# Kernel optimization log

Hardware: AMD Instinct MI355X
Metric: run time of the kernel (lower is better)

The kernel has to match this reference:

```python
import jax, jax.numpy as jnp
import numpy as np

N, K, D = 65536, 1024, 512


def setup_inputs() -> dict:
    key = jax.random.key(0)
    k1, k2, k3 = jax.random.split(key, 3)
    x = jax.random.normal(k1, (N, D), dtype=jnp.float32)
    y = jax.random.randint(k2, (N,), 0, K)  # true/assigned cluster labels
    centers = jax.random.normal(k3, (K, D), dtype=jnp.float32)  # nn.Parameter
    return {"x": x, "y": y, "centers": centers}


def reference(x, y, centers):
    # caldis: squared euclidean distance from every point to every center.
    # original expand+sub+square+sum without materializing [N, K, D]).
    x2 = jnp.sum(x * x, axis=1, keepdims=True)          # [N, 1]
    c2 = jnp.sum(centers * centers, axis=1)              # [K]
    distance = x2 - 2.0 * (x @ centers.T) + c2           # [N, K]

    # predict: torch.sort(distance)[1][:, 0] == index of the smallest distance
    ynew = jnp.argmin(distance, axis=1)                  # [N]

    # calwei + calloss: one-hot(y) * distance summed == gather distance[i, y[i]]
    loss = jnp.sum(jnp.take_along_axis(distance, y[:, None], axis=1))

    return loss, ynew
```

## Files before the change

### kernel.cpp

```cpp
#include <hip/hip_runtime.h>

#define NPTS 65536
#define KC   1024
#define DD   512

using bf16x8 = __attribute__((ext_vector_type(8))) __bf16;
using f32x4  = __attribute__((ext_vector_type(4))) float;

__device__ __forceinline__ void gld_lds16(const void* g, void* lds_base) {
  __builtin_amdgcn_global_load_lds(
      (const __attribute__((address_space(1))) unsigned int*)(uintptr_t)g,
      (__attribute__((address_space(3))) unsigned int*)(unsigned int)(uintptr_t)lds_base,
      16, 0, 0);
}

__device__ __forceinline__ uint2 pack4(const float4& v) {
  uint2 r;
  r.x = (__float_as_uint(v.x) >> 16) | (__float_as_uint(v.y) & 0xffff0000u);
  r.y = (__float_as_uint(v.z) >> 16) | (__float_as_uint(v.w) & 0xffff0000u);
  return r;
}


__global__ __launch_bounds__(256) void prep_kernel(
    const float* __restrict__ x, const int* __restrict__ y,
    const float* __restrict__ centers, uint4* __restrict__ xb,
    uint4* __restrict__ cbT, float* __restrict__ c2,
    float* __restrict__ partial) {
  const int w = threadIdx.x >> 6, l = threadIdx.x & 63;
  if (blockIdx.x >= 4096) {
    const int row = (blockIdx.x - 4096) * 4 + w;
    const float4* cf4 = (const float4*)centers;
    float4 a = cf4[row * 128 + 2 * l];
    float4 b = cf4[row * 128 + 2 * l + 1];
    uint2 pa = pack4(a), pb = pack4(b);
    cbT[(l >> 2) * 4096 + row * 4 + (l & 3)] = make_uint4(pa.x, pa.y, pb.x, pb.y);
    float s = a.x * a.x + a.y * a.y + a.z * a.z + a.w * a.w +
              b.x * b.x + b.y * b.y + b.z * b.z + b.w * b.w;
#pragma unroll
    for (int off = 32; off; off >>= 1) s += __shfl_down(s, off, 64);
    if (l == 0) c2[row] = s;
    return;
  }
  const int rbase = blockIdx.x * 16 + w * 4;
  const float4* xr = (const float4*)(x + (size_t)rbase * DD);
  float4 a[4], b[4];
#pragma unroll
  for (int r = 0; r < 4; r++) {
    a[r] = xr[r * 128 + 2 * l];
    b[r] = xr[r * 128 + 2 * l + 1];
  }
  int yr[4];
#pragma unroll
  for (int r = 0; r < 4; r++) yr[r] = y[rbase + r];
  float4 ca[4], cb4[4];
#pragma unroll
  for (int r = 0; r < 4; r++) {
    const float4* cr = (const float4*)(centers + (size_t)yr[r] * DD);
    ca[r]  = cr[2 * l];
    cb4[r] = cr[2 * l + 1];
  }
#pragma unroll
  for (int r = 0; r < 4; r++) {
    uint2 pa = pack4(a[r]), pb = pack4(b[r]);
    xb[(size_t)(rbase + r) * 64 + l] = make_uint4(pa.x, pa.y, pb.x, pb.y);
  }
  float s = 0.f;
#pragma unroll
  for (int r = 0; r < 4; r++) {
    float d0 = a[r].x - ca[r].x, d1 = a[r].y - ca[r].y;
    float d2 = a[r].z - ca[r].z, d3 = a[r].w - ca[r].w;
    float d4 = b[r].x - cb4[r].x, d5 = b[r].y - cb4[r].y;
    float d6 = b[r].z - cb4[r].z, d7 = b[r].w - cb4[r].w;
    s += d0 * d0 + d1 * d1 + d2 * d2 + d3 * d3 +
         d4 * d4 + d5 * d5 + d6 * d6 + d7 * d7;
  }
#pragma unroll
  for (int off = 32; off; off >>= 1) s += __shfl_down(s, off, 64);
  __shared__ float ps[4];
  if (l == 0) ps[w] = s;
  __syncthreads();
  if (threadIdx.x == 0) partial[blockIdx.x] = ps[0] + ps[1] + ps[2] + ps[3];
}

__global__ __launch_bounds__(512, 2) void gemm_argmin(
    const uint4* __restrict__ xb, const uint4* __restrict__ cbT,
    const float* __restrict__ c2, const float* __restrict__ partial,
    float* __restrict__ loss_out, float* __restrict__ ynew_out) {
  __shared__ uint4 As[8192];
  __shared__ float c2s[KC];
  __shared__ float ls[8];

  const int t = threadIdx.x;
  const int w = t >> 6, l = t & 63;
  const int wm = w >> 2, wn = w & 3;
  const int q4 = l >> 4, m16 = l & 15;
  const int row0 = blockIdx.x * 128;

  c2s[t] = c2[t];
  c2s[t + 512] = c2[t + 512];

  const int srow = l >> 2;
  const int schk = (l & 3) ^ ((l >> 3) & 3);
  const uint4* aB = xb + ((size_t)(row0 + w * 16 + srow) * 64 + schk);
  const int xs = q4 ^ ((m16 >> 1) & 3);
  const int al0 = (wm * 64 + m16) * 4 + xs;
  const int bl0 = (wn * 64 + m16) * 4 + q4;

#pragma unroll
  for (int p = 0; p < 4; p++)
    gld_lds16(aB + p * 4, &As[p * 512 + w * 64]);

  bf16x8 bA[4], bB[4];
#pragma unroll
  for (int j = 0; j < 4; j++)
    bA[j] = *(const bf16x8*)(cbT + bl0 + j * 64);

  f32x4 acc[4][4];
#pragma unroll
  for (int i = 0; i < 4; i++)
#pragma unroll
    for (int j = 0; j < 4; j++) acc[i][j] = (f32x4){0.f, 0.f, 0.f, 0.f};

  float best[16];
  int bi_[16];
#pragma unroll
  for (int i = 0; i < 16; i++) { best[i] = 3.4e38f; bi_[i] = 0; }

  asm volatile("s_waitcnt vmcnt(7)" ::: "memory");
  __builtin_amdgcn_s_barrier();

#define FOLD(P)                                                             \
  {                                                                         \
    const int n0f = (P) * 256;                                              \
    _Pragma("unroll")                                                       \
    for (int j = 0; j < 4; j++) {                                           \
      const int n = n0f + wn * 64 + j * 16 + m16;                           \
      const float cc = c2s[n];                                              \
      _Pragma("unroll")                                                     \
      for (int i = 0; i < 4; i++)                                           \
        _Pragma("unroll")                                                   \
        for (int r = 0; r < 4; r++) {                                       \
          float v = fmaf(-2.f, acc[i][j][r], cc);                           \
          const int bidx = i * 4 + r;                                       \
          if (v < best[bidx]) { best[bidx] = v; bi_[bidx] = n; }            \
          acc[i][j][r] = 0.f;                                               \
        }                                                                   \
    }                                                                       \
  }

#define TILE_P0(T, BC, BN)                                                  \
  {                                                                         \
    const int kt = (T) & 15;                                                \
    if ((T) < 15) {                                                         \
      const uint4* bp = cbT + ((T) + 1) * 4096;                             \
      _Pragma("unroll")                                                     \
      for (int j = 0; j < 4; j++)                                           \
        BN[j] = *(const bf16x8*)(bp + bl0 + j * 64);                        \
    }                                                                       \
    if ((T) < 12)                                                           \
      gld_lds16(aB + ((T) + 4) * 4, &As[((T) + 4) * 512 + w * 64]);         \
    bf16x8 af[4];                                                           \
    _Pragma("unroll")                                                       \
    for (int i = 0; i < 4; i++)                                             \
      af[i] = *(const bf16x8*)&As[kt * 512 + al0 + i * 64];                 \
    _Pragma("unroll")                                                       \
    for (int j = 0; j < 4; j++)                                             \
      _Pragma("unroll")                                                     \
      for (int i = 0; i < 4; i++)                                           \
        acc[i][j] = __builtin_amdgcn_mfma_f32_16x16x32_bf16(af[i], BC[j], acc[i][j], 0, 0, 0); \
    if ((T) == 15) FOLD(0);                                                 \
    if ((T) < 12) asm volatile("s_waitcnt vmcnt(1)" ::: "memory");          \
    else          asm volatile("s_waitcnt vmcnt(0)" ::: "memory");          \
    __builtin_amdgcn_s_barrier();                                           \
  }

#pragma unroll 1
  for (int s = 0; s < 8; ++s) {
    const int te = 2 * s;
    TILE_P0(te, bA, bB);
    TILE_P0(te + 1, bB, bA);
  }
#undef TILE_P0

#define TILE_MAIN(T, BC, BN)                                                \
  {                                                                         \
    const int kt = (T) & 15;                                                \
    if ((T) < 63) {                                                         \
      const int tn = (T) + 1;                                               \
      const uint4* bp = cbT + (tn & 15) * 4096 + ((tn >> 4) * 256) * 4;     \
      _Pragma("unroll")                                                     \
      for (int j = 0; j < 4; j++)                                           \
        BN[j] = *(const bf16x8*)(bp + bl0 + j * 64);                        \
    }                                                                       \
    bf16x8 af[4];                                                           \
    _Pragma("unroll")                                                       \
    for (int i = 0; i < 4; i++)                                             \
      af[i] = *(const bf16x8*)&As[kt * 512 + al0 + i * 64];                 \
    _Pragma("unroll")                                                       \
    for (int j = 0; j < 4; j++)                                             \
      _Pragma("unroll")                                                     \
      for (int i = 0; i < 4; i++)                                           \
        acc[i][j] = __builtin_amdgcn_mfma_f32_16x16x32_bf16(af[i], BC[j], acc[i][j], 0, 0, 0); \
    if (((T) & 15) == 15) FOLD((T) >> 4);                                   \
  }

#pragma unroll 1
  for (int s = 8; s < 32; ++s) {
    const int te = 2 * s;
    TILE_MAIN(te, bA, bB);
    TILE_MAIN(te + 1, bB, bA);
  }
#undef TILE_MAIN
#undef FOLD

  __syncthreads();

  float* mv = (float*)As;
  int*   mi = (int*)((char*)As + 2048);
#pragma unroll
  for (int bi = 0; bi < 16; bi++) {
    float v = best[bi];
    int idx = bi_[bi];
#pragma unroll
    for (int off = 8; off; off >>= 1) {
      float ov = __shfl_xor(v, off, 64);
      int oi = __shfl_xor(idx, off, 64);
      if (ov < v || (ov == v && oi < idx)) { v = ov; idx = oi; }
    }
    if (m16 == 0) {
      const int m = wm * 64 + (bi >> 2) * 16 + q4 * 4 + (bi & 3);
      mv[wn * 128 + m] = v;
      mi[wn * 128 + m] = idx;
    }
  }
  __syncthreads();
  if (t < 128) {
    float v = mv[t];
    int idx = mi[t];
#pragma unroll
    for (int p = 1; p < 4; p++) {
      float ov = mv[p * 128 + t];
      int oi = mi[p * 128 + t];
      if (ov < v || (ov == v && oi < idx)) { v = ov; idx = oi; }
    }
    ynew_out[row0 + t] = (float)idx;
  }

  if (blockIdx.x == 0) {
    float s = 0.f;
#pragma unroll
    for (int j = 0; j < 8; j++) s += partial[t + 512 * j];
#pragma unroll
    for (int off = 32; off; off >>= 1) s += __shfl_down(s, off, 64);
    if (l == 0) ls[w] = s;
    __syncthreads();
    if (t == 0) {
      float tot = 0.f;
#pragma unroll
      for (int i = 0; i < 8; i++) tot += ls[i];
      loss_out[0] = tot;
    }
  }
}

__global__ __launch_bounds__(256) void loss_final(const float* __restrict__ partial,
                                                  float* __restrict__ out) {
  float s = 0.f;
#pragma unroll
  for (int j = 0; j < 64; j++) s += partial[threadIdx.x + 256 * j];
#pragma unroll
  for (int off = 32; off; off >>= 1) s += __shfl_down(s, off, 64);
  __shared__ float ps[4];
  if ((threadIdx.x & 63) == 0) ps[threadIdx.x >> 6] = s;
  __syncthreads();
  if (threadIdx.x == 0) out[0] = ps[0] + ps[1] + ps[2] + ps[3];
}


#define SLOT(row, oct) (16 * (oct) + (((row) & 15) ^ (((oct) & 2) << 1)))

__device__ __forceinline__ void split_pack(const float4& a, const float4& b,
                                           uint4& hi, uint4& lo) {
  float f[8] = {a.x, a.y, a.z, a.w, b.x, b.y, b.z, b.w};
  uint hw[4], lw[4];
#pragma unroll
  for (int i = 0; i < 4; i++) {
    uint e0 = __float_as_uint(f[2 * i]), e1 = __float_as_uint(f[2 * i + 1]);
    hw[i] = (e0 >> 16) | (e1 & 0xffff0000u);
    float l0 = f[2 * i]     - __uint_as_float(e0 & 0xffff0000u);
    float l1 = f[2 * i + 1] - __uint_as_float(e1 & 0xffff0000u);
    lw[i] = (__float_as_uint(l0) >> 16) | (__float_as_uint(l1) & 0xffff0000u);
  }
  hi = make_uint4(hw[0], hw[1], hw[2], hw[3]);
  lo = make_uint4(lw[0], lw[1], lw[2], lw[3]);
}

__global__ __launch_bounds__(256) void c2_kernel(const float* __restrict__ centers,
                                                 float* __restrict__ c2) {
  int wave = (blockIdx.x * 256 + threadIdx.x) >> 6;
  int lane = threadIdx.x & 63;
  const float4* c4 = (const float4*)(centers + (size_t)wave * DD);
  float s = 0.f;
#pragma unroll
  for (int j = 0; j < 2; j++) {
    float4 v = c4[lane + 64 * j];
    s += v.x * v.x + v.y * v.y + v.z * v.z + v.w * v.w;
  }
#pragma unroll
  for (int off = 32; off; off >>= 1) s += __shfl_down(s, off, 64);
  if (lane == 0) c2[wave] = s;
}

__global__ __launch_bounds__(256, 2) void argmin_fb(
    const float* __restrict__ x, const float* __restrict__ centers,
    const float* __restrict__ c2, float* __restrict__ ynew_out) {
  __shared__ uint4 Ah[512], Al[512], Bh[512], Bl[512];
  const int t = threadIdx.x;
  const int w = t >> 6, l = t & 63;
  const int wm = w >> 1, wn = w & 1;
  const size_t row0 = (size_t)blockIdx.x * 128;
  const int srow = t >> 1, h = t & 1;
  const int mt = srow >> 4;
  const int so0 = mt * 64 + SLOT(srow, 2 * h);
  const int so1 = mt * 64 + SLOT(srow, 2 * h + 1);
  const int rs = SLOT(l & 15, l >> 4);
  const float* xp = x + (row0 + srow) * DD + h * 16;
  float best[16];
  int bidx[16];
#pragma unroll
  for (int i = 0; i < 16; i++) { best[i] = 3.4e38f; bidx[i] = 0; }
  for (int n0 = 0; n0 < KC; n0 += 128) {
    const float* bp = centers + (size_t)(n0 + srow) * DD + h * 16;
    f32x4 acc[4][4];
#pragma unroll
    for (int i = 0; i < 4; i++)
#pragma unroll
      for (int j = 0; j < 4; j++) acc[i][j] = (f32x4){0.f, 0.f, 0.f, 0.f};
    float4 ra[4], rb[4];
#pragma unroll
    for (int q = 0; q < 4; q++) {
      ra[q] = *(const float4*)(xp + q * 4);
      rb[q] = *(const float4*)(bp + q * 4);
    }
    for (int ks = 0; ks < 16; ks++) {
      uint4 ah0, al0, ah1, al1, bh0, bl0, bh1, bl1;
      split_pack(ra[0], ra[1], ah0, al0);
      split_pack(ra[2], ra[3], ah1, al1);
      split_pack(rb[0], rb[1], bh0, bl0);
      split_pack(rb[2], rb[3], bh1, bl1);
      __syncthreads();
      Ah[so0] = ah0; Al[so0] = al0;
      Ah[so1] = ah1; Al[so1] = al1;
      Bh[so0] = bh0; Bl[so0] = bl0;
      Bh[so1] = bh1; Bl[so1] = bl1;
      __syncthreads();
      if (ks < 15) {
#pragma unroll
        for (int q = 0; q < 4; q++) {
          ra[q] = *(const float4*)(xp + (ks + 1) * 32 + q * 4);
          rb[q] = *(const float4*)(bp + (ks + 1) * 32 + q * 4);
        }
      }
      bf16x8 afh[4], afl[4], bfh[4], bfl[4];
#pragma unroll
      for (int i = 0; i < 4; i++) {
        afh[i] = *(const bf16x8*)&Ah[(wm * 4 + i) * 64 + rs];
        afl[i] = *(const bf16x8*)&Al[(wm * 4 + i) * 64 + rs];
        bfh[i] = *(const bf16x8*)&Bh[(wn * 4 + i) * 64 + rs];
        bfl[i] = *(const bf16x8*)&Bl[(wn * 4 + i) * 64 + rs];
      }
#pragma unroll
      for (int i = 0; i < 4; i++)
#pragma unroll
        for (int j = 0; j < 4; j++) {
          acc[i][j] = __builtin_amdgcn_mfma_f32_16x16x32_bf16(afh[i], bfh[j], acc[i][j], 0, 0, 0);
          acc[i][j] = __builtin_amdgcn_mfma_f32_16x16x32_bf16(afl[i], bfh[j], acc[i][j], 0, 0, 0);
          acc[i][j] = __builtin_amdgcn_mfma_f32_16x16x32_bf16(afh[i], bfl[j], acc[i][j], 0, 0, 0);
        }
    }
#pragma unroll
    for (int j = 0; j < 4; j++) {
      int n = n0 + wn * 64 + j * 16 + (l & 15);
      float cc = c2[n];
#pragma unroll
      for (int i = 0; i < 4; i++)
#pragma unroll
        for (int r = 0; r < 4; r++) {
          float v = fmaf(-2.f, acc[i][j][r], cc);
          int bi = i * 4 + r;
          if (v < best[bi]) { best[bi] = v; bidx[bi] = n; }
        }
    }
  }
#pragma unroll
  for (int bi = 0; bi < 16; bi++) {
    float v = best[bi];
    int idx = bidx[bi];
#pragma unroll
    for (int off = 8; off; off >>= 1) {
      float ov = __shfl_xor(v, off, 64);
      int oi = __shfl_xor(idx, off, 64);
      if (ov < v || (ov == v && oi < idx)) { v = ov; idx = oi; }
    }
    if ((l & 15) == 0) {
      int m = wm * 64 + (bi >> 2) * 16 + (l >> 4) * 4 + (bi & 3);
      ynew_out[row0 + m] = (float)idx;
    }
  }
}

__global__ __launch_bounds__(256) void loss_partial_fb(
    const float* __restrict__ x, const int* __restrict__ y,
    const float* __restrict__ centers, float* __restrict__ partial) {
  const int w = threadIdx.x >> 6, l = threadIdx.x & 63;
  const int row = blockIdx.x * 4 + w;
  const float4* x4 = (const float4*)(x + (size_t)row * DD);
  const float4* c4 = (const float4*)(centers + (size_t)y[row] * DD);
  float s = 0.f;
#pragma unroll
  for (int j = 0; j < 2; j++) {
    float4 xv = x4[2 * l + j], cv = c4[2 * l + j];
    float dx = xv.x - cv.x, dy = xv.y - cv.y, dz = xv.z - cv.z, dw = xv.w - cv.w;
    s += dx * dx + dy * dy + dz * dz + dw * dw;
  }
#pragma unroll
  for (int off = 32; off; off >>= 1) s += __shfl_down(s, off, 64);
  __shared__ float ps[4];
  if (l == 0) ps[w] = s;
  __syncthreads();
  if (threadIdx.x == 0) partial[blockIdx.x] = ps[0] + ps[1] + ps[2] + ps[3];
}


extern "C" void kernel_launch(void* const* d_in, const int* in_sizes, int n_in,
                              void* d_out, int out_size, void* d_ws, size_t ws_size,
                              hipStream_t stream) {
  const float* x       = (const float*)d_in[0];
  const int*   y       = (const int*)d_in[1];
  const float* centers = (const float*)d_in[2];
  float* out = (float*)d_out;

  const size_t xb_bytes = (size_t)NPTS * DD * 2;
  const size_t cb_bytes = (size_t)KC * DD * 2;
  const size_t need = xb_bytes + cb_bytes + (KC + NPTS / 4) * sizeof(float);

  if (ws_size >= need) {
    uint4* xb      = (uint4*)d_ws;
    uint4* cbT     = (uint4*)((char*)d_ws + xb_bytes);
    float* c2      = (float*)((char*)d_ws + xb_bytes + cb_bytes);
    float* partial = c2 + KC;
    prep_kernel<<<4096 + 256, 256, 0, stream>>>(x, y, centers, xb, cbT, c2, partial);
    gemm_argmin<<<NPTS / 128, 512, 0, stream>>>(xb, cbT, c2, partial, out, out + 1);
  } else {
    float* c2      = (float*)d_ws;
    float* partial = c2 + KC;
    c2_kernel<<<KC / 4, 256, 0, stream>>>(centers, c2);
    argmin_fb<<<NPTS / 128, 256, 0, stream>>>(x, centers, c2, out + 1);
    loss_partial_fb<<<NPTS / 4, 256, 0, stream>>>(x, y, centers, partial);
    loss_final<<<1, 256, 0, stream>>>(partial, out);
  }
}
```

Measured before the change: 296.3 us.

## Restructure argmin GEMM to 4 waves with ring-buffered A tiles and packed min-index

Changes the GEMM-argmin kernel from 512 threads (2x4 wave grid, full A strip resident in LDS) to 256 threads, where each wave covers all 128 rows and 64 columns, giving a larger per-wave tile with more MFMA work per B fragment. A is now streamed through a 4-slot LDS ring buffer instead of being loaded fully up front, which reduces LDS use. The argmin tracking packs the center index into the low 10 mantissa bits of the distance so a single fminf replaces compare-and-select on separate value and index registers. The packing truncates mantissa bits and can pick a different index when distances are nearly tied, and the larger accumulator array raises register pressure.

New measurement: 274.3 us. 1.08x faster.

```diff
diff --git a/kernel.cpp b/kernel.cpp
--- a/kernel.cpp
+++ b/kernel.cpp
@@ -83,184 +83,140 @@
   if (threadIdx.x == 0) partial[blockIdx.x] = ps[0] + ps[1] + ps[2] + ps[3];
 }
 
-__global__ __launch_bounds__(512, 2) void gemm_argmin(
+__global__ __launch_bounds__(256, 2) void gemm_argmin(
     const uint4* __restrict__ xb, const uint4* __restrict__ cbT,
     const float* __restrict__ c2, const float* __restrict__ partial,
     float* __restrict__ loss_out, float* __restrict__ ynew_out) {
-  __shared__ uint4 As[8192];
+  __shared__ uint4 As[2048];
   __shared__ float c2s[KC];
-  __shared__ float ls[8];
+  __shared__ float ls[4];
 
   const int t = threadIdx.x;
   const int w = t >> 6, l = t & 63;
-  const int wm = w >> 2, wn = w & 3;
   const int q4 = l >> 4, m16 = l & 15;
   const int row0 = blockIdx.x * 128;
 
-  c2s[t] = c2[t];
-  c2s[t + 512] = c2[t + 512];
+#pragma unroll
+  for (int i = 0; i < 4; i++) c2s[t + 256 * i] = c2[t + 256 * i];
 
   const int srow = l >> 2;
   const int schk = (l & 3) ^ ((l >> 3) & 3);
-  const uint4* aB = xb + ((size_t)(row0 + w * 16 + srow) * 64 + schk);
+  const uint4* aBlo = xb + ((size_t)(row0 + w * 32 + srow) * 64 + schk);
+  const uint4* aBhi = aBlo + 16 * 64;
   const int xs = q4 ^ ((m16 >> 1) & 3);
-  const int al0 = (wm * 64 + m16) * 4 + xs;
-  const int bl0 = (wn * 64 + m16) * 4 + q4;
-
-#pragma unroll
-  for (int p = 0; p < 4; p++)
-    gld_lds16(aB + p * 4, &As[p * 512 + w * 64]);
-
+  const int bl0 = w * 256 + m16 * 4 + q4;
+
+#pragma unroll
+  for (int p = 0; p < 3; p++) {
+    gld_lds16(aBlo + p * 4, &As[p * 512 + w * 128]);
+    gld_lds16(aBhi + p * 4, &As[p * 512 + w * 128 + 64]);
+  }
   bf16x8 bA[4], bB[4];
 #pragma unroll
   for (int j = 0; j < 4; j++)
     bA[j] = *(const bf16x8*)(cbT + bl0 + j * 64);
 
-  f32x4 acc[4][4];
-#pragma unroll
-  for (int i = 0; i < 4; i++)
+  f32x4 acc[8][4];
+#pragma unroll
+  for (int i = 0; i < 8; i++)
 #pragma unroll
     for (int j = 0; j < 4; j++) acc[i][j] = (f32x4){0.f, 0.f, 0.f, 0.f};
 
-  float best[16];
-  int bi_[16];
-#pragma unroll
-  for (int i = 0; i < 16; i++) { best[i] = 3.4e38f; bi_[i] = 0; }
-
-  asm volatile("s_waitcnt vmcnt(7)" ::: "memory");
+  float best[32];
+#pragma unroll
+  for (int i = 0; i < 32; i++) best[i] = 3.4e38f;
+
+  asm volatile("s_waitcnt vmcnt(8)" ::: "memory");
   __builtin_amdgcn_s_barrier();
 
 #define FOLD(P)                                                             \
   {                                                                         \
-    const int n0f = (P) * 256;                                              \
     _Pragma("unroll")                                                       \
     for (int j = 0; j < 4; j++) {                                           \
-      const int n = n0f + wn * 64 + j * 16 + m16;                           \
+      const int n = (P) * 256 + w * 64 + j * 16 + m16;                      \
       const float cc = c2s[n];                                              \
       _Pragma("unroll")                                                     \
-      for (int i = 0; i < 4; i++)                                           \
+      for (int i = 0; i < 8; i++)                                           \
         _Pragma("unroll")                                                   \
         for (int r = 0; r < 4; r++) {                                       \
           float v = fmaf(-2.f, acc[i][j][r], cc);                           \
-          const int bidx = i * 4 + r;                                       \
-          if (v < best[bidx]) { best[bidx] = v; bi_[bidx] = n; }            \
+          uint pk = (__float_as_uint(v) & 0xFFFFFC00u) | (uint)n;           \
+          const int bx = i * 4 + r;                                         \
+          best[bx] = fminf(best[bx], __uint_as_float(pk));                  \
           acc[i][j][r] = 0.f;                                               \
         }                                                                   \
     }                                                                       \
   }
 
-#define TILE_P0(T, BC, BN)                                                  \
+#define TILE(T, BC, BN)                                                     \
   {                                                                         \
-    const int kt = (T) & 15;                                                \
-    if ((T) < 15) {                                                         \
-      const uint4* bp = cbT + ((T) + 1) * 4096;                             \
+    const int bse = ((T) & 3) * 512;                                        \
+    if ((T) < 63) {              \
+      const int tn = (T) + 1;                                               \
+      const uint4* bp = cbT + (tn & 15) * 4096 + (tn >> 4) * 1024;          \
       _Pragma("unroll")                                                     \
       for (int j = 0; j < 4; j++)                                           \
         BN[j] = *(const bf16x8*)(bp + bl0 + j * 64);                        \
     }                                                                       \
-    if ((T) < 12)                                                           \
-      gld_lds16(aB + ((T) + 4) * 4, &As[((T) + 4) * 512 + w * 64]);         \
-    bf16x8 af[4];                                                           \
+    if ((T) <= 60) {                      \
+      const int s2 = (((T) + 3) & 3) * 512;                                 \
+      const int oa = (((T) + 3) & 15) * 4;                                  \
+      gld_lds16(aBlo + oa, &As[s2 + w * 128]);                              \
+      gld_lds16(aBhi + oa, &As[s2 + w * 128 + 64]);                         \
+    }                                                                       \
     _Pragma("unroll")                                                       \
-    for (int i = 0; i < 4; i++)                                             \
-      af[i] = *(const bf16x8*)&As[kt * 512 + al0 + i * 64];                 \
-    _Pragma("unroll")                                                       \
-    for (int j = 0; j < 4; j++)                                             \
-      _Pragma("unroll")                                                     \
-      for (int i = 0; i < 4; i++)                                           \
-        acc[i][j] = __builtin_amdgcn_mfma_f32_16x16x32_bf16(af[i], BC[j], acc[i][j], 0, 0, 0); \
-    if ((T) == 15) FOLD(0);                                                 \
-    if ((T) < 12) asm volatile("s_waitcnt vmcnt(1)" ::: "memory");          \
-    else          asm volatile("s_waitcnt vmcnt(0)" ::: "memory");          \
-    __builtin_amdgcn_s_barrier();                                           \
-  }
-
-#pragma unroll 1
-  for (int s = 0; s < 8; ++s) {
-    const int te = 2 * s;
-    TILE_P0(te, bA, bB);
-    TILE_P0(te + 1, bB, bA);
-  }
-#undef TILE_P0
-
-#define TILE_MAIN(T, BC, BN)                                                \
-  {                                                                         \
-    const int kt = (T) & 15;                                                \
-    if ((T) < 63) {                                                         \
-      const int tn = (T) + 1;                                               \
-      const uint4* bp = cbT + (tn & 15) * 4096 + ((tn >> 4) * 256) * 4;     \
+    for (int i = 0; i < 8; i++) {                                           \
+      bf16x8 af = *(const bf16x8*)&As[bse + (i * 16 + m16) * 4 + xs];       \
       _Pragma("unroll")                                                     \
       for (int j = 0; j < 4; j++)                                           \
-        BN[j] = *(const bf16x8*)(bp + bl0 + j * 64);                        \
+        acc[i][j] = __builtin_amdgcn_mfma_f32_16x16x32_bf16(af, BC[j], acc[i][j], 0, 0, 0); \
     }                                                                       \
-    bf16x8 af[4];                                                           \
-    _Pragma("unroll")                                                       \
-    for (int i = 0; i < 4; i++)                                             \
-      af[i] = *(const bf16x8*)&As[kt * 512 + al0 + i * 64];                 \
-    _Pragma("unroll")                                                       \
-    for (int j = 0; j < 4; j++)                                             \
-      _Pragma("unroll")                                                     \
-      for (int i = 0; i < 4; i++)                                           \
-        acc[i][j] = __builtin_amdgcn_mfma_f32_16x16x32_bf16(af[i], BC[j], acc[i][j], 0, 0, 0); \
     if (((T) & 15) == 15) FOLD((T) >> 4);                                   \
+    if ((T) <= 60)      asm volatile("s_waitcnt vmcnt(8)" ::: "memory");    \
+    else if ((T) == 61) asm volatile("s_waitcnt vmcnt(6)" ::: "memory");    \
+    else if ((T) == 62) asm volatile("s_waitcnt vmcnt(4)" ::: "memory");    \
+    if ((T) < 63) __builtin_amdgcn_s_barrier();                             \
   }
 
 #pragma unroll 1
-  for (int s = 8; s < 32; ++s) {
+  for (int s = 0; s < 32; ++s) {
     const int te = 2 * s;
-    TILE_MAIN(te, bA, bB);
-    TILE_MAIN(te + 1, bB, bA);
-  }
-#undef TILE_MAIN
+    TILE(te, bA, bB);
+    TILE(te + 1, bB, bA);
+  }
+#undef TILE
 #undef FOLD
 
   __syncthreads();
 
   float* mv = (float*)As;
-  int*   mi = (int*)((char*)As + 2048);
-#pragma unroll
-  for (int bi = 0; bi < 16; bi++) {
+#pragma unroll
+  for (int bi = 0; bi < 32; bi++) {
     float v = best[bi];
-    int idx = bi_[bi];
-#pragma unroll
-    for (int off = 8; off; off >>= 1) {
-      float ov = __shfl_xor(v, off, 64);
-      int oi = __shfl_xor(idx, off, 64);
-      if (ov < v || (ov == v && oi < idx)) { v = ov; idx = oi; }
-    }
+#pragma unroll
+    for (int off = 8; off; off >>= 1) v = fminf(v, __shfl_xor(v, off, 64));
     if (m16 == 0) {
-      const int m = wm * 64 + (bi >> 2) * 16 + q4 * 4 + (bi & 3);
-      mv[wn * 128 + m] = v;
-      mi[wn * 128 + m] = idx;
+      const int row = (bi >> 2) * 16 + q4 * 4 + (bi & 3);
+      mv[w * 128 + row] = v;
     }
   }
   __syncthreads();
   if (t < 128) {
-    float v = mv[t];
-    int idx = mi[t];
-#pragma unroll
-    for (int p = 1; p < 4; p++) {
-      float ov = mv[p * 128 + t];
-      int oi = mi[p * 128 + t];
-      if (ov < v || (ov == v && oi < idx)) { v = ov; idx = oi; }
-    }
-    ynew_out[row0 + t] = (float)idx;
+    float v = fminf(fminf(mv[t], mv[128 + t]), fminf(mv[256 + t], mv[384 + t]));
+    ynew_out[row0 + t] = (float)(__float_as_uint(v) & 1023u);
   }
 
   if (blockIdx.x == 0) {
     float s = 0.f;
 #pragma unroll
-    for (int j = 0; j < 8; j++) s += partial[t + 512 * j];
+    for (int j = 0; j < 16; j++) s += partial[t + 256 * j];
 #pragma unroll
     for (int off = 32; off; off >>= 1) s += __shfl_down(s, off, 64);
     if (l == 0) ls[w] = s;
     __syncthreads();
-    if (t == 0) {
-      float tot = 0.f;
-#pragma unroll
-      for (int i = 0; i < 8; i++) tot += ls[i];
-      loss_out[0] = tot;
-    }
+    if (t == 0) ls[0] = ls[0] + ls[1] + ls[2] + ls[3];
+    __syncthreads();
+    if (t == 0) loss_out[0] = ls[0];
   }
 }
 
@@ -451,7 +407,7 @@
     float* c2      = (float*)((char*)d_ws + xb_bytes + cb_bytes);
     float* partial = c2 + KC;
     prep_kernel<<<4096 + 256, 256, 0, stream>>>(x, y, centers, xb, cbT, c2, partial);
-    gemm_argmin<<<NPTS / 128, 512, 0, stream>>>(xb, cbT, c2, partial, out, out + 1);
+    gemm_argmin<<<NPTS / 128, 256, 0, stream>>>(xb, cbT, c2, partial, out, out + 1);
   } else {
     float* c2      = (float*)d_ws;
     float* partial = c2 + KC;
```
